# Kernel tuning notes

Hardware: AMD Instinct MI355X
Metric: run time of the kernel (lower is better)

Reference implementation:

```python
import jax, jax.numpy as jnp
import numpy as np

B, A, D, H = 2, 512, 512, 8
HD = D // H
SCALE = HD ** -0.5
REL_HID = 512


def _layernorm(x, g, b, eps=1e-5):
    m = jnp.mean(x, axis=-1, keepdims=True)
    v = jnp.var(x, axis=-1, keepdims=True)
    return (x - m) * jax.lax.rsqrt(v + eps) * g + b


def setup_inputs() -> dict:
    key = jax.random.key(0)
    ks = jax.random.split(key, 12)
    s = 0.02
    return {
        "x": jax.random.normal(ks[0], (B, A, D), jnp.float32),
        "mask": jax.random.bernoulli(ks[1], 0.1, (B, A)),
        "relation": jax.random.normal(ks[2], (B, A, A, 4), jnp.float32),
        "qkv_w": jax.random.normal(ks[3], (D, 3 * D), jnp.float32) * s,
        "qkv_b": jnp.zeros((3 * D,), jnp.float32),
        "rel_w1": jax.random.normal(ks[4], (4, REL_HID), jnp.float32) * s,
        "rel_b1": jnp.zeros((REL_HID,), jnp.float32),
        "rel_w2": jax.random.normal(ks[5], (REL_HID, H), jnp.float32) * s,
        "ff_w1": jax.random.normal(ks[6], (D, 3 * D), jnp.float32) * s,
        "ff_b1": jnp.zeros((3 * D,), jnp.float32),
        "ff_w2": jax.random.normal(ks[7], (3 * D, D), jnp.float32) * s,
        "ff_b2": jnp.zeros((D,), jnp.float32),
        "ln1_g": jnp.ones((D,), jnp.float32),
        "ln1_b": jnp.zeros((D,), jnp.float32),
        "ln2_g": jnp.ones((D,), jnp.float32),
        "ln2_b": jnp.zeros((D,), jnp.float32),
    }


def reference(x, mask, relation, qkv_w, qkv_b, rel_w1, rel_b1, rel_w2,
              ff_w1, ff_b1, ff_w2, ff_b2, ln1_g, ln1_b, ln2_g, ln2_b):
    b, a, d = x.shape
    res_attn = x
    qkv = (x @ qkv_w + qkv_b).reshape(b, a, 3, H, HD).transpose(2, 0, 3, 1, 4)
    q, k, v = qkv[0] * SCALE, qkv[1], qkv[2]          # (B,H,A,HD)
    attn = jnp.einsum('bhid,bhjd->bhij', q, k)        # (B,H,A,A)
    # per-head relation bias from MLP on pairwise relations
    rel_emb = jax.nn.relu(relation @ rel_w1 + rel_b1) @ rel_w2  # (B,A,A,H)
    attn = attn + 16.0 * jax.nn.sigmoid(rel_emb.transpose(0, 3, 1, 2))
    # key-side mask: -inf where mask is True
    attn = attn + jnp.where(mask, -1e9, 0.0).astype(attn.dtype)[:, None, None, :]
    attn = jax.nn.softmax(attn, axis=-1)
    out = jnp.einsum('bhij,bhjd->bhid', attn, v).transpose(0, 2, 1, 3).reshape(b, a, d)
    x1 = _layernorm(out + res_attn, ln1_g, ln1_b)
    ff = jax.nn.relu(x1 @ ff_w1 + ff_b1) @ ff_w2 + ff_b2
    return _layernorm(x1 + ff, ln2_g, ln2_b)
```

## Files before the change

kernel.cpp:

```cpp
#include <hip/hip_runtime.h>
#include <hip/hip_bf16.h>

#define A_  512
#define D_  512
#define H_  8
#define HD_ 64
#define TD_ 1536
#define RH_ 512

typedef __attribute__((ext_vector_type(8))) short short8v;
typedef __attribute__((ext_vector_type(4))) float f32x4;
typedef __attribute__((ext_vector_type(4))) unsigned int u32x4;
union V8 { u32x4 u; short8v s; };

__device__ __forceinline__ unsigned short f2bf(float f) {
    unsigned int u = __float_as_uint(f);
    u += 0x7FFFu + ((u >> 16) & 1u);
    return (unsigned short)(u >> 16);
}
__device__ __forceinline__ float bf2f(unsigned short v) {
    return __uint_as_float((unsigned)v << 16);
}
__device__ __forceinline__ unsigned pk2(float a, float b) {
    unsigned r;
    asm("v_cvt_pk_bf16_f32 %0, %1, %2" : "=v"(r) : "v"(a), "v"(b));
    return r;
}
__device__ __forceinline__ unsigned pk2r(float a, float b) {
    return pk2(fmaxf(a, 0.f), fmaxf(b, 0.f));
}

__global__ __launch_bounds__(256) void prep_kernel(const float* __restrict__ x,
                                                   const void* __restrict__ mraw,
                                                   ushort* __restrict__ xb,
                                                   float* __restrict__ maskf) {
    const int tid = threadIdx.x;
    if (blockIdx.x == 256) {
        __shared__ int anyOdd;
        if (tid == 0) anyOdd = 0;
        __syncthreads();
        const unsigned char* mb = (const unsigned char*)mraw;
        int local = 0;
        #pragma unroll
        for (int u = 0; u < 4; ++u) {
            const int i = tid * 4 + u;
            if ((i & 3) != 0 && mb[i] != 0) local = 1;
        }
        if (local) atomicOr(&anyOdd, 1);
        __syncthreads();
        const bool isByte = (anyOdd != 0);
        #pragma unroll
        for (int u = 0; u < 4; ++u) {
            const int i = tid * 4 + u;
            int set = isByte ? (mb[i] != 0) : (((const int*)mraw)[i] != 0);
            maskf[i] = set ? -1e9f : 0.0f;
        }
        return;
    }
    const int i = (blockIdx.x * 256 + tid) * 8;
    const float4 a = *(const float4*)&x[i];
    const float4 b = *(const float4*)&x[i + 4];
    uint4 o;
    o.x = pk2(a.x, a.y);
    o.y = pk2(a.z, a.w);
    o.z = pk2(b.x, b.y);
    o.w = pk2(b.z, b.w);
    *(uint4*)&xb[i] = o;
}

__device__ __forceinline__ void wt_body(const float* __restrict__ in,
                                        ushort* __restrict__ out,
                                        int R, int C, int bx, int by) {
    __shared__ float ts[64][65];
    const int tid = threadIdx.x;
    const int r0 = by * 64, c0 = bx * 64;
    const int r = tid >> 2, cb = (tid & 3) * 16;
    #pragma unroll
    for (int u = 0; u < 4; ++u) {
        const float4 v = *(const float4*)&in[(size_t)(r0 + r) * C + c0 + cb + u*4];
        ts[r][cb + u*4 + 0] = v.x;
        ts[r][cb + u*4 + 1] = v.y;
        ts[r][cb + u*4 + 2] = v.z;
        ts[r][cb + u*4 + 3] = v.w;
    }
    __syncthreads();
    const int oc = tid & 63;
    const int rb = (tid >> 6) * 16;
    unsigned pk[8];
    #pragma unroll
    for (int i = 0; i < 8; ++i) {
        pk[i] = pk2(ts[rb + i*2][oc], ts[rb + i*2 + 1][oc]);
    }
    uint4* dst = (uint4*)&out[(size_t)(c0 + oc) * R + r0 + rb];
    dst[0] = make_uint4(pk[0], pk[1], pk[2], pk[3]);
    dst[1] = make_uint4(pk[4], pk[5], pk[6], pk[7]);
}

__global__ __launch_bounds__(256) void wt3_kernel(const float* __restrict__ qkv_w,
                                                  const float* __restrict__ ff_w1,
                                                  const float* __restrict__ ff_w2,
                                                  ushort* __restrict__ wtb1,
                                                  ushort* __restrict__ wtb2,
                                                  ushort* __restrict__ wtb3) {
    const int bid = blockIdx.x;
    if (bid < 192) {
        wt_body(qkv_w, wtb1, 512, 1536, bid % 24, bid / 24);
    } else if (bid < 384) {
        const int i = bid - 192;
        wt_body(ff_w1, wtb2, 512, 1536, i % 24, i / 24);
    } else {
        const int i = bid - 384;
        wt_body(ff_w2, wtb3, 1536, 512, i % 8, i / 8);
    }
}

template<int RELU, int OBF16, int SCALEQ>
__global__ __launch_bounds__(256) void mgemm_kernel(const ushort* __restrict__ A,
                                                    const ushort* __restrict__ BT,
                                                    const float* __restrict__ bias,
                                                    void* __restrict__ Cv,
                                                    int M, int N, int K) {
    __shared__ __align__(16) ushort As[64 * 64];
    __shared__ __align__(16) ushort Bs[64 * 64];
    const int tid = threadIdx.x;
    const int bm = blockIdx.y * 64, bn = blockIdx.x * 64;
    const int lane = tid & 63, wave = tid >> 6;
    const int wm = (wave >> 1) * 32, wn = (wave & 1) * 32;
    f32x4 acc[2][2];
    #pragma unroll
    for (int i = 0; i < 2; ++i)
        #pragma unroll
        for (int j = 0; j < 2; ++j) acc[i][j] = (f32x4){0.f, 0.f, 0.f, 0.f};

    const int s0  = tid * 2;
    const int rs  = s0 >> 3;
    const int sl0 = s0 & 7;
    for (int k0 = 0; k0 < K; k0 += 64) {
        #pragma unroll
        for (int u = 0; u < 2; ++u) {
            const int sl = sl0 + u;
            const uint4 va = *(const uint4*)&A[(size_t)(bm + rs) * K + k0 + sl*8];
            *(uint4*)((char*)As + rs*128 + ((sl ^ (rs & 7)) << 4)) = va;
            const uint4 vb = *(const uint4*)&BT[(size_t)(bn + rs) * K + k0 + sl*8];
            *(uint4*)((char*)Bs + rs*128 + ((sl ^ (rs & 7)) << 4)) = vb;
        }
        __syncthreads();
        #pragma unroll
        for (int kk = 0; kk < 2; ++kk) {
            short8v af[2], bfv[2];
            #pragma unroll
            for (int mf = 0; mf < 2; ++mf) {
                const int row = wm + mf*16 + (lane & 15);
                const int slot = (kk*4 + (lane >> 4)) ^ (row & 7);
                af[mf] = *(const short8v*)((const char*)As + row*128 + (slot << 4));
            }
            #pragma unroll
            for (int nf = 0; nf < 2; ++nf) {
                const int row = wn + nf*16 + (lane & 15);
                const int slot = (kk*4 + (lane >> 4)) ^ (row & 7);
                bfv[nf] = *(const short8v*)((const char*)Bs + row*128 + (slot << 4));
            }
            #pragma unroll
            for (int mf = 0; mf < 2; ++mf)
                #pragma unroll
                for (int nf = 0; nf < 2; ++nf)
                    acc[mf][nf] = __builtin_amdgcn_mfma_f32_16x16x32_bf16(af[mf], bfv[nf], acc[mf][nf], 0, 0, 0);
        }
        __syncthreads();
    }
    #pragma unroll
    for (int nf = 0; nf < 2; ++nf) {
        const int col = bn + wn + nf*16 + (lane & 15);
        const float bv = bias[col];
        const float qs = (SCALEQ && col < D_) ? 0.125f : 1.0f;
        #pragma unroll
        for (int mf = 0; mf < 2; ++mf) {
            #pragma unroll
            for (int r = 0; r < 4; ++r) {
                const int row = bm + wm + mf*16 + (lane >> 4)*4 + r;
                float v = acc[mf][nf][r] + bv;
                if (RELU) v = fmaxf(v, 0.f);
                if (SCALEQ) v *= qs;
                if (OBF16) ((ushort*)Cv)[(size_t)row * N + col] = f2bf(v);
                else       ((float*)Cv)[(size_t)row * N + col] = v;
            }
        }
    }
}

__global__ __launch_bounds__(256) void relmlp_kernel(const float* __restrict__ rel,
                                                     const float* __restrict__ w1,
                                                     const float* __restrict__ b1,
                                                     const float* __restrict__ w2,
                                                     const float* __restrict__ maskf,
                                                     ushort* __restrict__ relbM) {
    __shared__ __align__(16) ushort w1t[512 * 8];
    __shared__ __align__(16) ushort w2t[8 * 512];
    const int tid = threadIdx.x;
    #pragma unroll
    for (int u = 0; u < 2; ++u) {
        const int n = tid + u*256;
        uint4 o;
        o.x = (unsigned)f2bf(w1[n])        | ((unsigned)f2bf(w1[512 + n])  << 16);
        o.y = (unsigned)f2bf(w1[1024 + n]) | ((unsigned)f2bf(w1[1536 + n]) << 16);
        o.z = (unsigned)f2bf(b1[n]);
        o.w = 0;
        *(uint4*)&w1t[n * 8] = o;
        const int ch = n >> 5, w = n & 31, t = w >> 4, i = w & 15;
        const int s = ((i >> 2) << 3) + (t << 2) + (i & 3);
        const int kpos = ch * 32 + s;
        const float4 wlo = *(const float4*)&w2[n*8];
        const float4 whi = *(const float4*)&w2[n*8 + 4];
        const float wvv[8] = {wlo.x, wlo.y, wlo.z, wlo.w, whi.x, whi.y, whi.z, whi.w};
        #pragma unroll
        for (int h = 0; h < 8; ++h) {
            *(ushort*)((char*)w2t + h*1024 + (((kpos >> 3) ^ h) << 4) + (kpos & 7)*2) = f2bf(wvv[h]);
        }
    }
    __syncthreads();

    const int lane = tid & 63, wvid = tid >> 6;
    const int g = lane >> 4, lr = lane & 15;
    const f32x4 z4 = {0.f, 0.f, 0.f, 0.f};
    const int pbase = blockIdx.x * 256 + wvid * 64;

    short8v rf[4];
    #pragma unroll
    for (int pt = 0; pt < 4; ++pt) {
        short8v r8 = {0,0,0,0,0,0,0,0};
        if (g == 0) {
            const float4 ra = *(const float4*)&rel[(size_t)(pbase + pt*16 + lr) * 4];
            r8[0] = (short)f2bf(ra.x); r8[1] = (short)f2bf(ra.y);
            r8[2] = (short)f2bf(ra.z); r8[3] = (short)f2bf(ra.w);
            r8[4] = (short)0x3F80;
        }
        rf[pt] = r8;
    }
    f32x4 acc[4];
    #pragma unroll
    for (int pt = 0; pt < 4; ++pt) acc[pt] = z4;

    #pragma unroll 2
    for (int ch = 0; ch < 16; ++ch) {
        short8v a2 = {0,0,0,0,0,0,0,0};
        if (lr < 8) a2 = *(const short8v*)((const char*)w2t + lr*1024 + (((ch*4 + g) ^ lr) << 4));
        short8v af0 = {0,0,0,0,0,0,0,0}, af1 = {0,0,0,0,0,0,0,0};
        if (g == 0) {
            af0 = *(const short8v*)&w1t[(ch*32 + lr) * 8];
            af1 = *(const short8v*)&w1t[(ch*32 + 16 + lr) * 8];
        }
        #pragma unroll
        for (int pt = 0; pt < 4; ++pt) {
            const f32x4 c0 = __builtin_amdgcn_mfma_f32_16x16x32_bf16(af0, rf[pt], z4, 0, 0, 0);
            const f32x4 c1 = __builtin_amdgcn_mfma_f32_16x16x32_bf16(af1, rf[pt], z4, 0, 0, 0);
            V8 bfrag;
            bfrag.u.x = pk2r(c0[0], c0[1]); bfrag.u.y = pk2r(c0[2], c0[3]);
            bfrag.u.z = pk2r(c1[0], c1[1]); bfrag.u.w = pk2r(c1[2], c1[3]);
            acc[pt] = __builtin_amdgcn_mfma_f32_16x16x32_bf16(a2, bfrag.s, acc[pt], 0, 0, 0);
        }
    }
    if (g < 2) {
        #pragma unroll
        for (int pt = 0; pt < 4; ++pt) {
            const int pair = pbase + pt*16 + lr;
            const int bb_  = pair >> 18;
            const int ij   = pair & 262143;
            const float mv = maskf[bb_ * A_ + (pair & 511)];
            ushort* dst = relbM + (((size_t)(bb_ * 8)) << 18) + ij;
            #pragma unroll
            for (int r = 0; r < 4; ++r) {
                const int h = g*4 + r;
                dst[(size_t)h << 18] = f2bf(16.0f / (1.0f + __expf(-acc[pt][r])) + mv);
            }
        }
    }
}

__global__ __launch_bounds__(256) void vt_kernel(const ushort* __restrict__ qkvb,
                                                 ushort* __restrict__ VT) {
    const int bh = blockIdx.y, jt = blockIdx.x;
    const int b = bh >> 3, h = bh & 7;
    __shared__ ushort ts[64][72];
    const int tid = threadIdx.x;
    const int r = tid >> 2, c16 = (tid & 3) * 16;
    const ushort* src = qkvb + (size_t)(b*A_ + jt*64 + r) * TD_ + 2*D_ + h*HD_ + c16;
    *(uint4*)&ts[r][c16]     = *(const uint4*)&src[0];
    *(uint4*)&ts[r][c16 + 8] = *(const uint4*)&src[8];
    __syncthreads();
    const int d = tid >> 2, jb = (tid & 3) * 16;
    unsigned pk[8];
    #pragma unroll
    for (int i = 0; i < 8; ++i)
        pk[i] = (unsigned)ts[jb + i*2][d] | ((unsigned)ts[jb + i*2 + 1][d] << 16);
    uint4* dst = (uint4*)&VT[(size_t)(bh*64 + d) * A_ + jt*64 + jb];
    dst[0] = make_uint4(pk[0], pk[1], pk[2], pk[3]);
    dst[1] = make_uint4(pk[4], pk[5], pk[6], pk[7]);
}

__global__ __launch_bounds__(64) void attn_kernel(const ushort* __restrict__ qkvb,
                                                  const ushort* __restrict__ relbM,
                                                  const ushort* __restrict__ vtb,
                                                  float* __restrict__ outb) {
    const int blk = blockIdx.x;
    const int bh = blk >> 5, it = blk & 31;
    const int b = bh >> 3, h = bh & 7;
    const int i0 = it * 16;
    const int lane = threadIdx.x;
    const int g = lane >> 4, lr = lane & 15;
    __shared__ __align__(16) ushort Pl[16 * 512];

    const ushort* Qrow = qkvb + (size_t)(b*A_ + i0 + lr) * TD_ + h*HD_;
    const short8v qf0 = *(const short8v*)&Qrow[g*8];
    const short8v qf1 = *(const short8v*)&Qrow[32 + g*8];

    const ushort* Kbase = qkvb + (size_t)(b*A_) * TD_ + D_ + h*HD_;
    f32x4 s[32];
    #pragma unroll
    for (int jt = 0; jt < 32; ++jt) {
        const ushort* Krow = Kbase + (size_t)(jt*16 + lr) * TD_;
        const short8v a0 = *(const short8v*)&Krow[g*8];
        const short8v a1 = *(const short8v*)&Krow[32 + g*8];
        f32x4 c = {0.f, 0.f, 0.f, 0.f};
        c = __builtin_amdgcn_mfma_f32_16x16x32_bf16(a0, qf0, c, 0, 0, 0);
        c = __builtin_amdgcn_mfma_f32_16x16x32_bf16(a1, qf1, c, 0, 0, 0);
        s[jt] = c;
    }
    const ushort* rb = relbM + ((size_t)bh << 18) + (size_t)(i0 + lr) * A_;
    #pragma unroll
    for (int jt = 0; jt < 32; ++jt) {
        const uint2 m2 = *(const uint2*)&rb[jt*16 + g*4];
        s[jt][0] += __uint_as_float(m2.x << 16);
        s[jt][1] += __uint_as_float(m2.x & 0xFFFF0000u);
        s[jt][2] += __uint_as_float(m2.y << 16);
        s[jt][3] += __uint_as_float(m2.y & 0xFFFF0000u);
    }
    float mx = -3.0e38f;
    #pragma unroll
    for (int jt = 0; jt < 32; ++jt)
        mx = fmaxf(mx, fmaxf(fmaxf(s[jt][0], s[jt][1]), fmaxf(s[jt][2], s[jt][3])));
    mx = fmaxf(mx, __shfl_xor(mx, 16));
    mx = fmaxf(mx, __shfl_xor(mx, 32));
    float sum = 0.f;
    #pragma unroll
    for (int jt = 0; jt < 32; ++jt) {
        #pragma unroll
        for (int r = 0; r < 4; ++r) {
            const float e = __expf(s[jt][r] - mx);
            s[jt][r] = e;
            sum += e;
        }
    }
    sum += __shfl_xor(sum, 16);
    sum += __shfl_xor(sum, 32);
    const float inv = 1.0f / sum;
    char* Plc = (char*)Pl;
    #pragma unroll
    for (int jt = 0; jt < 32; ++jt) {
        uint2 w;
        w.x = pk2(s[jt][0] * inv, s[jt][1] * inv);
        w.y = pk2(s[jt][2] * inv, s[jt][3] * inv);
        const int j0 = jt*16 + g*4;
        *(uint2*)(Plc + lr*1024 + (((j0 >> 3) ^ (lr & 7)) << 4) + (j0 & 7)*2) = w;
    }
    __syncthreads();
    f32x4 o[4];
    #pragma unroll
    for (int dt = 0; dt < 4; ++dt) o[dt] = (f32x4){0.f, 0.f, 0.f, 0.f};
    const ushort* Vb = vtb + (size_t)bh * 64 * A_;
    #pragma unroll
    for (int c = 0; c < 16; ++c) {
        const short8v pa = *(const short8v*)(Plc + lr*1024 + (((c*4 + g) ^ (lr & 7)) << 4));
        #pragma unroll
        for (int dt = 0; dt < 4; ++dt) {
            const short8v vf = *(const short8v*)&Vb[(size_t)(dt*16 + lr) * A_ + c*32 + g*8];
            o[dt] = __builtin_amdgcn_mfma_f32_16x16x32_bf16(pa, vf, o[dt], 0, 0, 0);
        }
    }
    float* Ob = outb + (size_t)(b*A_ + i0) * D_ + h*HD_;
    #pragma unroll
    for (int dt = 0; dt < 4; ++dt)
        #pragma unroll
        for (int r = 0; r < 4; ++r)
            Ob[(size_t)(g*4 + r) * D_ + dt*16 + lr] = o[dt][r];
}

template<int BF16OUT>
__global__ __launch_bounds__(256) void ln_kernel(const float* __restrict__ a,
                                                 const float* __restrict__ r,
                                                 const float* __restrict__ g,
                                                 const float* __restrict__ bb,
                                                 float* __restrict__ out,
                                                 ushort* __restrict__ outb) {
    const int row = blockIdx.x;
    const int tid = threadIdx.x;
    const size_t base = (size_t)row * D_ + tid * 2;
    const float2 a2 = *reinterpret_cast<const float2*>(&a[base]);
    const float2 r2 = *reinterpret_cast<const float2*>(&r[base]);
    const float e0 = a2.x + r2.x, e1 = a2.y + r2.y;
    float s = e0 + e1;
    float q = e0*e0 + e1*e1;
    #pragma unroll
    for (int o = 32; o > 0; o >>= 1) { s += __shfl_down(s, o); q += __shfl_down(q, o); }
    __shared__ float rs[4], rq[4];
    if ((tid & 63) == 0) { rs[tid >> 6] = s; rq[tid >> 6] = q; }
    __syncthreads();
    const float S = rs[0]+rs[1]+rs[2]+rs[3];
    const float Q = rq[0]+rq[1]+rq[2]+rq[3];
    const float mean = S * (1.0f/512.0f);
    const float var  = Q * (1.0f/512.0f) - mean*mean;
    const float rstd = rsqrtf(var + 1e-5f);
    const int c = tid*2;
    float2 ov;
    ov.x = (e0 - mean)*rstd*g[c]   + bb[c];
    ov.y = (e1 - mean)*rstd*g[c+1] + bb[c+1];
    *reinterpret_cast<float2*>(&out[base]) = ov;
    if (BF16OUT) {
        *(unsigned*)&outb[base] = pk2(ov.x, ov.y);
    }
}

extern "C" void kernel_launch(void* const* d_in, const int* in_sizes, int n_in,
                              void* d_out, int out_size, void* d_ws, size_t ws_size,
                              hipStream_t stream) {
    const float* x        = (const float*)d_in[0];
    const void*  mask     = d_in[1];
    const float* relation = (const float*)d_in[2];
    const float* qkv_w    = (const float*)d_in[3];
    const float* qkv_b    = (const float*)d_in[4];
    const float* rel_w1   = (const float*)d_in[5];
    const float* rel_b1   = (const float*)d_in[6];
    const float* rel_w2   = (const float*)d_in[7];
    const float* ff_w1    = (const float*)d_in[8];
    const float* ff_b1    = (const float*)d_in[9];
    const float* ff_w2    = (const float*)d_in[10];
    const float* ff_b2    = (const float*)d_in[11];
    const float* ln1_g    = (const float*)d_in[12];
    const float* ln1_b    = (const float*)d_in[13];
    const float* ln2_g    = (const float*)d_in[14];
    const float* ln2_b    = (const float*)d_in[15];
    float* out = (float*)d_out;

    float* ws     = (float*)d_ws;
    ushort* relbM = (ushort*)ws;
    float*  maskf = (float*)(relbM + 4194304);
    float*  attnb = maskf + 1024;
    float*  x1    = attnb + 524288;
    ushort* wtb1  = (ushort*)(x1 + 524288);
    ushort* wtb2  = wtb1 + 786432;
    ushort* wtb3  = wtb2 + 786432;
    ushort* xb    = wtb3 + 786432;
    ushort* ffhb  = xb  + 524288;
    ushort* qkvb  = ffhb + 1572864;
    ushort* vtb   = qkvb + 1572864;
    float*  ff2o  = (float*)qkvb;
    ushort* x1b   = xb;

    prep_kernel<<<257, 256, 0, stream>>>(x, mask, xb, maskf);
    wt3_kernel<<<576, 256, 0, stream>>>(qkv_w, ff_w1, ff_w2, wtb1, wtb2, wtb3);
    mgemm_kernel<0,1,1><<<dim3(24, 16), 256, 0, stream>>>(xb, wtb1, qkv_b, qkvb, 1024, 1536, 512);
    relmlp_kernel<<<2048, 256, 0, stream>>>(relation, rel_w1, rel_b1, rel_w2, maskf, relbM);
    vt_kernel<<<dim3(8, 16), 256, 0, stream>>>(qkvb, vtb);
    attn_kernel<<<512, 64, 0, stream>>>(qkvb, relbM, vtb, attnb);
    ln_kernel<1><<<1024, 256, 0, stream>>>(attnb, x, ln1_g, ln1_b, x1, x1b);
    mgemm_kernel<1,1,0><<<dim3(24, 16), 256, 0, stream>>>(x1b, wtb2, ff_b1, ffhb, 1024, 1536, 512);
    mgemm_kernel<0,0,0><<<dim3(8, 16), 256, 0, stream>>>(ffhb, wtb3, ff_b2, ff2o, 1024, 512, 1536);
    ln_kernel<0><<<1024, 256, 0, stream>>>(ff2o, x1, ln2_g, ln2_b, out, nullptr);
}
```

Measured before the change: 115.8 us.

## Merge prep/weight-transpose kernels and fuse QKV GEMM with relation MLP launch

Combines the input conversion, mask build and three weight transposes into one launch. It also runs the QKV GEMM and the relation-MLP bias computation as disjoint block ranges of a single kernel. The aim is to remove launch gaps and let the small GEMM overlap with the large relmlp work. The relmlp inner loop drops its per-lane conditional LDS loads in favour of unconditional loads, which trades wasted lanes for extra LDS traffic. The fused kernel's register use and occupancy are set by the heavier of the two bodies.

```diff
diff --git a/kernel.cpp b/kernel.cpp
--- a/kernel.cpp
+++ b/kernel.cpp
@@ -18,9 +18,6 @@
     u += 0x7FFFu + ((u >> 16) & 1u);
     return (unsigned short)(u >> 16);
 }
-__device__ __forceinline__ float bf2f(unsigned short v) {
-    return __uint_as_float((unsigned)v << 16);
-}
 __device__ __forceinline__ unsigned pk2(float a, float b) {
     unsigned r;
     asm("v_cvt_pk_bf16_f32 %0, %1, %2" : "=v"(r) : "v"(a), "v"(b));
@@ -30,48 +27,10 @@
     return pk2(fmaxf(a, 0.f), fmaxf(b, 0.f));
 }
 
-__global__ __launch_bounds__(256) void prep_kernel(const float* __restrict__ x,
-                                                   const void* __restrict__ mraw,
-                                                   ushort* __restrict__ xb,
-                                                   float* __restrict__ maskf) {
-    const int tid = threadIdx.x;
-    if (blockIdx.x == 256) {
-        __shared__ int anyOdd;
-        if (tid == 0) anyOdd = 0;
-        __syncthreads();
-        const unsigned char* mb = (const unsigned char*)mraw;
-        int local = 0;
-        #pragma unroll
-        for (int u = 0; u < 4; ++u) {
-            const int i = tid * 4 + u;
-            if ((i & 3) != 0 && mb[i] != 0) local = 1;
-        }
-        if (local) atomicOr(&anyOdd, 1);
-        __syncthreads();
-        const bool isByte = (anyOdd != 0);
-        #pragma unroll
-        for (int u = 0; u < 4; ++u) {
-            const int i = tid * 4 + u;
-            int set = isByte ? (mb[i] != 0) : (((const int*)mraw)[i] != 0);
-            maskf[i] = set ? -1e9f : 0.0f;
-        }
-        return;
-    }
-    const int i = (blockIdx.x * 256 + tid) * 8;
-    const float4 a = *(const float4*)&x[i];
-    const float4 b = *(const float4*)&x[i + 4];
-    uint4 o;
-    o.x = pk2(a.x, a.y);
-    o.y = pk2(a.z, a.w);
-    o.z = pk2(b.x, b.y);
-    o.w = pk2(b.z, b.w);
-    *(uint4*)&xb[i] = o;
-}
-
-__device__ __forceinline__ void wt_body(const float* __restrict__ in,
+__device__ __forceinline__ void wt_body(float (*ts)[65],
+                                        const float* __restrict__ in,
                                         ushort* __restrict__ out,
                                         int R, int C, int bx, int by) {
-    __shared__ float ts[64][65];
     const int tid = threadIdx.x;
     const int r0 = by * 64, c0 = bx * 64;
     const int r = tid >> 2, cb = (tid & 3) * 16;
@@ -96,34 +55,69 @@
     dst[1] = make_uint4(pk[4], pk[5], pk[6], pk[7]);
 }
 
-__global__ __launch_bounds__(256) void wt3_kernel(const float* __restrict__ qkv_w,
-                                                  const float* __restrict__ ff_w1,
-                                                  const float* __restrict__ ff_w2,
-                                                  ushort* __restrict__ wtb1,
-                                                  ushort* __restrict__ wtb2,
-                                                  ushort* __restrict__ wtb3) {
+__global__ __launch_bounds__(256) void prep2_kernel(const float* __restrict__ x,
+                                                    const void* __restrict__ mraw,
+                                                    const float* __restrict__ qkv_w,
+                                                    const float* __restrict__ ff_w1,
+                                                    const float* __restrict__ ff_w2,
+                                                    ushort* __restrict__ xb,
+                                                    float* __restrict__ maskf,
+                                                    ushort* __restrict__ wtb1,
+                                                    ushort* __restrict__ wtb2,
+                                                    ushort* __restrict__ wtb3) {
+    __shared__ __align__(16) float ts[64][65];
+    const int tid = threadIdx.x;
     const int bid = blockIdx.x;
-    if (bid < 192) {
-        wt_body(qkv_w, wtb1, 512, 1536, bid % 24, bid / 24);
-    } else if (bid < 384) {
-        const int i = bid - 192;
-        wt_body(ff_w1, wtb2, 512, 1536, i % 24, i / 24);
+    if (bid < 256) {
+        const int i = (bid * 256 + tid) * 8;
+        const float4 a = *(const float4*)&x[i];
+        const float4 b = *(const float4*)&x[i + 4];
+        uint4 o;
+        o.x = pk2(a.x, a.y);
+        o.y = pk2(a.z, a.w);
+        o.z = pk2(b.x, b.y);
+        o.w = pk2(b.z, b.w);
+        *(uint4*)&xb[i] = o;
+    } else if (bid == 256) {
+        int* anyOdd = (int*)ts;
+        if (tid == 0) *anyOdd = 0;
+        __syncthreads();
+        const unsigned char* mb = (const unsigned char*)mraw;
+        int local = 0;
+        #pragma unroll
+        for (int u = 0; u < 4; ++u) {
+            const int i = tid * 4 + u;
+            if ((i & 3) != 0 && mb[i] != 0) local = 1;
+        }
+        if (local) atomicOr(anyOdd, 1);
+        __syncthreads();
+        const bool isByte = (*anyOdd != 0);
+        #pragma unroll
+        for (int u = 0; u < 4; ++u) {
+            const int i = tid * 4 + u;
+            int set = isByte ? (mb[i] != 0) : (((const int*)mraw)[i] != 0);
+            maskf[i] = set ? -1e9f : 0.0f;
+        }
+    } else if (bid < 449) {
+        const int i = bid - 257;
+        wt_body(ts, qkv_w, wtb1, 512, 1536, i % 24, i / 24);
+    } else if (bid < 641) {
+        const int i = bid - 449;
+        wt_body(ts, ff_w1, wtb2, 512, 1536, i % 24, i / 24);
     } else {
-        const int i = bid - 384;
-        wt_body(ff_w2, wtb3, 1536, 512, i % 8, i / 8);
+        const int i = bid - 641;
+        wt_body(ts, ff_w2, wtb3, 1536, 512, i % 8, i / 8);
     }
 }
 
 template<int RELU, int OBF16, int SCALEQ>
-__global__ __launch_bounds__(256) void mgemm_kernel(const ushort* __restrict__ A,
-                                                    const ushort* __restrict__ BT,
-                                                    const float* __restrict__ bias,
-                                                    void* __restrict__ Cv,
-                                                    int M, int N, int K) {
-    __shared__ __align__(16) ushort As[64 * 64];
-    __shared__ __align__(16) ushort Bs[64 * 64];
-    const int tid = threadIdx.x;
-    const int bm = blockIdx.y * 64, bn = blockIdx.x * 64;
+__device__ __forceinline__ void mgemm_body(ushort* As, ushort* Bs,
+                                           const ushort* __restrict__ A,
+                                           const ushort* __restrict__ BT,
+                                           const float* __restrict__ bias,
+                                           void* __restrict__ Cv,
+                                           int N, int K, int bm, int bn) {
+    const int tid = threadIdx.x;
     const int lane = tid & 63, wave = tid >> 6;
     const int wm = (wave >> 1) * 32, wn = (wave & 1) * 32;
     f32x4 acc[2][2];
@@ -188,14 +182,26 @@
     }
 }
 
-__global__ __launch_bounds__(256) void relmlp_kernel(const float* __restrict__ rel,
-                                                     const float* __restrict__ w1,
-                                                     const float* __restrict__ b1,
-                                                     const float* __restrict__ w2,
-                                                     const float* __restrict__ maskf,
-                                                     ushort* __restrict__ relbM) {
-    __shared__ __align__(16) ushort w1t[512 * 8];
-    __shared__ __align__(16) ushort w2t[8 * 512];
+template<int RELU, int OBF16, int SCALEQ>
+__global__ __launch_bounds__(256) void mgemm_kernel(const ushort* __restrict__ A,
+                                                    const ushort* __restrict__ BT,
+                                                    const float* __restrict__ bias,
+                                                    void* __restrict__ Cv,
+                                                    int M, int N, int K) {
+    __shared__ __align__(16) ushort As[64 * 64];
+    __shared__ __align__(16) ushort Bs[64 * 64];
+    mgemm_body<RELU, OBF16, SCALEQ>(As, Bs, A, BT, bias, Cv, N, K,
+                                    blockIdx.y * 64, blockIdx.x * 64);
+}
+
+__device__ __forceinline__ void relmlp_body(ushort* w1t, ushort* w2t,
+                                            const float* __restrict__ rel,
+                                            const float* __restrict__ w1,
+                                            const float* __restrict__ b1,
+                                            const float* __restrict__ w2,
+                                            const float* __restrict__ maskf,
+                                            ushort* __restrict__ relbM,
+                                            int bid) {
     const int tid = threadIdx.x;
     #pragma unroll
     for (int u = 0; u < 2; ++u) {
@@ -222,7 +228,7 @@
     const int lane = tid & 63, wvid = tid >> 6;
     const int g = lane >> 4, lr = lane & 15;
     const f32x4 z4 = {0.f, 0.f, 0.f, 0.f};
-    const int pbase = blockIdx.x * 256 + wvid * 64;
+    const int pbase = bid * 256 + wvid * 64;
 
     short8v rf[4];
     #pragma unroll
@@ -242,13 +248,9 @@
 
     #pragma unroll 2
     for (int ch = 0; ch < 16; ++ch) {
-        short8v a2 = {0,0,0,0,0,0,0,0};
-        if (lr < 8) a2 = *(const short8v*)((const char*)w2t + lr*1024 + (((ch*4 + g) ^ lr) << 4));
-        short8v af0 = {0,0,0,0,0,0,0,0}, af1 = {0,0,0,0,0,0,0,0};
-        if (g == 0) {
-            af0 = *(const short8v*)&w1t[(ch*32 + lr) * 8];
-            af1 = *(const short8v*)&w1t[(ch*32 + 16 + lr) * 8];
-        }
+        const short8v a2  = *(const short8v*)((const char*)w2t + (lr & 7)*1024 + (((ch*4 + g) ^ (lr & 7)) << 4));
+        const short8v af0 = *(const short8v*)&w1t[(ch*32 + lr) * 8];
+        const short8v af1 = *(const short8v*)&w1t[(ch*32 + 16 + lr) * 8];
         #pragma unroll
         for (int pt = 0; pt < 4; ++pt) {
             const f32x4 c0 = __builtin_amdgcn_mfma_f32_16x16x32_bf16(af0, rf[pt], z4, 0, 0, 0);
@@ -273,6 +275,28 @@
                 dst[(size_t)h << 18] = f2bf(16.0f / (1.0f + __expf(-acc[pt][r])) + mv);
             }
         }
+    }
+}
+
+__global__ __launch_bounds__(256) void fused_qr_kernel(const ushort* __restrict__ xb,
+                                                       const ushort* __restrict__ wtb1,
+                                                       const float* __restrict__ qkv_b,
+                                                       ushort* __restrict__ qkvb,
+                                                       const float* __restrict__ rel,
+                                                       const float* __restrict__ w1,
+                                                       const float* __restrict__ b1,
+                                                       const float* __restrict__ w2,
+                                                       const float* __restrict__ maskf,
+                                                       ushort* __restrict__ relbM) {
+    __shared__ __align__(16) char smem[16384];
+    const int bid = blockIdx.x;
+    if (bid < 384) {
+        mgemm_body<0, 1, 1>((ushort*)smem, (ushort*)(smem + 8192),
+                            xb, wtb1, qkv_b, qkvb, 1536, 512,
+                            (bid / 24) * 64, (bid % 24) * 64);
+    } else {
+        relmlp_body((ushort*)smem, (ushort*)(smem + 8192),
+                    rel, w1, b1, w2, maskf, relbM, bid - 384);
     }
 }
 
@@ -455,10 +479,11 @@
     float*  ff2o  = (float*)qkvb;
     ushort* x1b   = xb;
 
-    prep_kernel<<<257, 256, 0, stream>>>(x, mask, xb, maskf);
-    wt3_kernel<<<576, 256, 0, stream>>>(qkv_w, ff_w1, ff_w2, wtb1, wtb2, wtb3);
-    mgemm_kernel<0,1,1><<<dim3(24, 16), 256, 0, stream>>>(xb, wtb1, qkv_b, qkvb, 1024, 1536, 512);
-    relmlp_kernel<<<2048, 256, 0, stream>>>(relation, rel_w1, rel_b1, rel_w2, maskf, relbM);
+    prep2_kernel<<<833, 256, 0, stream>>>(x, mask, qkv_w, ff_w1, ff_w2,
+                                          xb, maskf, wtb1, wtb2, wtb3);
+    fused_qr_kernel<<<2432, 256, 0, stream>>>(xb, wtb1, qkv_b, qkvb,
+                                              relation, rel_w1, rel_b1, rel_w2,
+                                              maskf, relbM);
     vt_kernel<<<dim3(8, 16), 256, 0, stream>>>(qkvb, vtb);
     attn_kernel<<<512, 64, 0, stream>>>(qkvb, relbM, vtb, attnb);
     ln_kernel<1><<<1024, 256, 0, stream>>>(attnb, x, ln1_g, ln1_b, x1, x1b);
```

Result: faster. 103.6 us (median of 2 runs) (-10.5%).
